# Kernel tuning notes

Measured on AMD Instinct MI355X. Metric: run time of the kernel, lower is better.

Reference implementation:

```python
import jax, jax.numpy as jnp
import numpy as np

B, S, E, H, V, C = 64, 512, 256, 128, 50000, 2


def setup_inputs() -> dict:
    key = jax.random.key(0)
    ks = jax.random.split(key, 12)
    sentences = jax.random.randint(ks[0], (B, S), 0, V, dtype=jnp.int32)
    # sparse binary adjacency (dependency-tree-like), float for bmm
    adj = (jax.random.uniform(ks[1], (B, S, S)) < 0.05).astype(jnp.float32)
    emb_table = jax.random.normal(ks[2], (V, E), dtype=jnp.float32) * 0.02
    W1 = jax.random.normal(ks[3], (H, E), dtype=jnp.float32) * 0.05
    b1 = jnp.zeros((H,), jnp.float32)
    W2 = jax.random.normal(ks[4], (H, H), dtype=jnp.float32) * 0.05
    b2 = jnp.zeros((H,), jnp.float32)
    W3 = jax.random.normal(ks[5], (H, H), dtype=jnp.float32) * 0.05
    b3 = jnp.zeros((H,), jnp.float32)
    Wp = jax.random.normal(ks[6], (C, H), dtype=jnp.float32) * 0.05
    bp = jnp.zeros((C,), jnp.float32)
    return {"sentences": sentences, "adj": adj, "emb_table": emb_table,
            "W1": W1, "b1": b1, "W2": W2, "b2": b2, "W3": W3, "b3": b3,
            "Wp": Wp, "bp": bp}


def reference(sentences, adj, emb_table, W1, b1, W2, b2, W3, b3, Wp, bp):
    # embedding lookup (dropout is eval-mode identity)
    h = emb_table[sentences]  # [B, S, E]
    # degree normalization term (self-loop adds +1)
    deg = jnp.sum(adj, axis=-1, keepdims=True) + 1.0  # [B, S, 1]
    for W, b in ((W1, b1), (W2, b2), (W3, b3)):
        agg = jnp.einsum('bst,btd->bsd', adj, h)  # bmm(adj, h)
        # layer(agg) + layer(h) == (agg + h) @ W^T + 2b  (shared weights)
        h = ((agg + h) @ W.T + 2.0 * b) / deg
        h = jax.nn.relu(h)
    # AdaptiveMaxPool1d(1) over sequence dim
    pooled = jnp.max(h, axis=1)  # [B, H]
    logits = pooled @ Wp.T + bp  # [B, C]
    return logits
```

## Files before the change

### kernel.cpp

```cpp
#include <hip/hip_runtime.h>
#include <hip/hip_bf16.h>

typedef unsigned short ushort_t;

#define B_ 64
#define S_ 512
#define E_ 256
#define H_ 128
#define M_ (B_ * S_)
#define CAP_ 128

__global__ void k_adjidx(const float* __restrict__ adj,
                         ushort_t* __restrict__ idxl,
                         int* __restrict__ nnz,
                         float* __restrict__ invdeg) {
    int row  = blockIdx.x * 4 + (threadIdx.x >> 6);
    int lane = threadIdx.x & 63;
    const float* arow = adj + (size_t)row * S_;
    int total = 0;
    #pragma unroll
    for (int c = 0; c < 8; ++c) {
        float v = arow[c * 64 + lane];
        unsigned long long m = __ballot(v != 0.0f);
        if (v != 0.0f) {
            int pos = total + __popcll(m & ((1ull << lane) - 1ull));
            if (pos < CAP_) idxl[(size_t)row * CAP_ + pos] = (ushort_t)(c * 64 + lane);
        }
        total += __popcll(m);
    }
    if (lane == 0) {
        nnz[row] = total < CAP_ ? total : CAP_;
        invdeg[row] = 1.0f / (float)(total + 1);
    }
}

template <int KDIM, bool GATHER>
__global__ __launch_bounds__(256) void k_gemm(const float* __restrict__ X,
                                              const int* __restrict__ sent,
                                              const float* __restrict__ emb,
                                              const float* __restrict__ W,
                                              float* __restrict__ out) {
    const int BK = 16;
    __shared__ float Xs[BK][68];
    __shared__ float Ws[BK][132];
    int tid = threadIdx.x;
    int rowBlock = blockIdx.x * 64;
    int r0 = (tid >> 5) * 8;
    int c0 = (tid & 31) * 4;
    float acc[8][4] = {};

    int mIdx = tid >> 2;
    int k4   = (tid & 3) * 4;
    const float* xsrc;
    if (GATHER) xsrc = emb + (size_t)sent[rowBlock + mIdx] * KDIM + k4;
    else        xsrc = X   + (size_t)(rowBlock + mIdx) * KDIM + k4;
    int wj = tid >> 1;
    int k8 = (tid & 1) * 8;
    const float* wsrc = W + (size_t)wj * KDIM + k8;

    for (int kk = 0; kk < KDIM; kk += BK) {
        float4 xf = *(const float4*)(xsrc + kk);
        float4 w0 = *(const float4*)(wsrc + kk);
        float4 w1 = *(const float4*)(wsrc + kk + 4);
        Xs[k4 + 0][mIdx] = xf.x; Xs[k4 + 1][mIdx] = xf.y;
        Xs[k4 + 2][mIdx] = xf.z; Xs[k4 + 3][mIdx] = xf.w;
        Ws[k8 + 0][wj] = w0.x; Ws[k8 + 1][wj] = w0.y;
        Ws[k8 + 2][wj] = w0.z; Ws[k8 + 3][wj] = w0.w;
        Ws[k8 + 4][wj] = w1.x; Ws[k8 + 5][wj] = w1.y;
        Ws[k8 + 6][wj] = w1.z; Ws[k8 + 7][wj] = w1.w;
        __syncthreads();
        #pragma unroll
        for (int k = 0; k < BK; ++k) {
            float4 a0 = *(const float4*)&Xs[k][r0];
            float4 a1 = *(const float4*)&Xs[k][r0 + 4];
            float4 wv = *(const float4*)&Ws[k][c0];
            float xv[8] = {a0.x, a0.y, a0.z, a0.w, a1.x, a1.y, a1.z, a1.w};
            #pragma unroll
            for (int i = 0; i < 8; ++i) {
                acc[i][0] += xv[i] * wv.x;
                acc[i][1] += xv[i] * wv.y;
                acc[i][2] += xv[i] * wv.z;
                acc[i][3] += xv[i] * wv.w;
            }
        }
        __syncthreads();
    }

    #pragma unroll
    for (int i = 0; i < 8; ++i) {
        int row = rowBlock + r0 + i;
        float4 o = {acc[i][0], acc[i][1], acc[i][2], acc[i][3]};
        *(float4*)(out + (size_t)row * H_ + c0) = o;
    }
}

__global__ __launch_bounds__(256) void k_aggf(const float* __restrict__ Y,
                                              const ushort_t* __restrict__ idxl,
                                              const int* __restrict__ nnz,
                                              const float* __restrict__ invdeg,
                                              const float* __restrict__ bias,
                                              float* __restrict__ out) {
    int x    = blockIdx.x;
    int xcd  = x & 7;
    int slot = x >> 3;
    int b    = xcd + 8 * (slot >> 6);
    int g    = slot & 63;
    int row  = b * S_ + g * 8 + (threadIdx.x >> 5);
    int c    = threadIdx.x & 31;

    const float4* Y4 = (const float4*)Y;
    int n = nnz[row];
    const ushort_t* il = idxl + (size_t)row * CAP_;
    float4 acc = Y4[(size_t)row * 32 + c];
    float4 acc2 = {0.f, 0.f, 0.f, 0.f};
    size_t base = (size_t)b * S_ * 32;

    int i = 0;
    for (; i + 4 <= n; i += 4) {
        int t0 = il[i], t1 = il[i + 1], t2 = il[i + 2], t3 = il[i + 3];
        float4 v0 = Y4[base + (size_t)t0 * 32 + c];
        float4 v1 = Y4[base + (size_t)t1 * 32 + c];
        float4 v2 = Y4[base + (size_t)t2 * 32 + c];
        float4 v3 = Y4[base + (size_t)t3 * 32 + c];
        acc.x += v0.x + v1.x; acc.y += v0.y + v1.y;
        acc.z += v0.z + v1.z; acc.w += v0.w + v1.w;
        acc2.x += v2.x + v3.x; acc2.y += v2.y + v3.y;
        acc2.z += v2.z + v3.z; acc2.w += v2.w + v3.w;
    }
    for (; i < n; ++i) {
        int t = il[i];
        float4 v = Y4[base + (size_t)t * 32 + c];
        acc.x += v.x; acc.y += v.y; acc.z += v.z; acc.w += v.w;
    }
    acc.x += acc2.x; acc.y += acc2.y; acc.z += acc2.z; acc.w += acc2.w;

    float inv = invdeg[row];
    float4 bv = ((const float4*)bias)[c];
    float4 o;
    o.x = fmaxf((acc.x + 2.0f * bv.x) * inv, 0.0f);
    o.y = fmaxf((acc.y + 2.0f * bv.y) * inv, 0.0f);
    o.z = fmaxf((acc.z + 2.0f * bv.z) * inv, 0.0f);
    o.w = fmaxf((acc.w + 2.0f * bv.w) * inv, 0.0f);
    ((float4*)out)[(size_t)row * 32 + c] = o;
}

__global__ void k_pool(const float* __restrict__ h, float* __restrict__ pp) {
    int b = blockIdx.x, sb = blockIdx.y, j = threadIdx.x;
    const float* p = h + ((size_t)b * S_ + sb * 64) * H_ + j;
    float m = -1e30f;
    #pragma unroll 8
    for (int s = 0; s < 64; ++s) m = fmaxf(m, p[(size_t)s * H_]);
    pp[((size_t)b * 8 + sb) * H_ + j] = m;
}

__global__ void k_final(const float* __restrict__ pp,
                        const float* __restrict__ Wp,
                        const float* __restrict__ bp,
                        float* __restrict__ out) {
    int b = blockIdx.x, j = threadIdx.x;
    float m = -1e30f;
    #pragma unroll
    for (int i = 0; i < 8; ++i) m = fmaxf(m, pp[((size_t)b * 8 + i) * H_ + j]);
    float t0 = m * Wp[j];
    float t1 = m * Wp[H_ + j];
    #pragma unroll
    for (int off = 32; off > 0; off >>= 1) {
        t0 += __shfl_down(t0, off);
        t1 += __shfl_down(t1, off);
    }
    __shared__ float red[2][2];
    int wave = j >> 6, lane = j & 63;
    if (lane == 0) { red[0][wave] = t0; red[1][wave] = t1; }
    __syncthreads();
    if (j == 0) out[b * 2 + 0] = red[0][0] + red[0][1] + bp[0];
    if (j == 1) out[b * 2 + 1] = red[1][0] + red[1][1] + bp[1];
}

extern "C" void kernel_launch(void* const* d_in, const int* in_sizes, int n_in,
                              void* d_out, int out_size, void* d_ws, size_t ws_size,
                              hipStream_t stream) {
    const int*   sent = (const int*)d_in[0];
    const float* adj  = (const float*)d_in[1];
    const float* emb  = (const float*)d_in[2];
    const float* W1   = (const float*)d_in[3];
    const float* b1   = (const float*)d_in[4];
    const float* W2   = (const float*)d_in[5];
    const float* b2   = (const float*)d_in[6];
    const float* W3   = (const float*)d_in[7];
    const float* b3   = (const float*)d_in[8];
    const float* Wp   = (const float*)d_in[9];
    const float* bp   = (const float*)d_in[10];
    float* out = (float*)d_out;

    char* ws = (char*)d_ws;
    float*    bufA   = (float*)ws;
    float*    bufB   = (float*)(ws + (size_t)M_ * 256 * 4);
    float*    invdeg = (float*)(ws + (size_t)M_ * 512 * 4);
    int*      nnz    = (int*)(ws + (size_t)M_ * 512 * 4 + M_ * 4);
    ushort_t* idxl   = (ushort_t*)(ws + (size_t)M_ * 512 * 4 + M_ * 8);
    float*    pp     = (float*)(ws + (size_t)M_ * 512 * 4 + M_ * 8 + (size_t)M_ * CAP_ * 2);

    k_adjidx<<<M_ / 4, 256, 0, stream>>>(adj, idxl, nnz, invdeg);

    k_gemm<E_, true><<<M_ / 64, 256, 0, stream>>>(nullptr, sent, emb, W1, bufA);
    k_aggf<<<M_ / 8, 256, 0, stream>>>(bufA, idxl, nnz, invdeg, b1, bufB);

    k_gemm<H_, false><<<M_ / 64, 256, 0, stream>>>(bufB, nullptr, nullptr, W2, bufA);
    k_aggf<<<M_ / 8, 256, 0, stream>>>(bufA, idxl, nnz, invdeg, b2, bufB);

    k_gemm<H_, false><<<M_ / 64, 256, 0, stream>>>(bufB, nullptr, nullptr, W3, bufA);
    k_aggf<<<M_ / 8, 256, 0, stream>>>(bufA, idxl, nnz, invdeg, b3, bufB);

    k_pool <<<dim3(B_, 8), H_, 0, stream>>>(bufB, pp);
    k_final<<<B_, H_, 0, stream>>>(pp, Wp, bp, out);
}
```

Baseline: 314.3 us.

## Fuse max-pool into final aggregation, double-buffer GEMM smem, vectorize adjacency scan

The last aggregation kernel now reduces each 8-row block to a partial max and writes it directly, so the full layer-3 activations are never stored and the separate pool kernel is removed; the final kernel reduces 64 partials instead of 8. The GEMM uses double-buffered shared memory with register prefetch of the next tile, dropping one barrier per K-step. The adjacency index builder reads float4 per lane instead of scalars. The larger partial buffer requires more workspace, and the register prefetch adds register pressure.

```diff
diff --git a/kernel.cpp b/kernel.cpp
--- a/kernel.cpp
+++ b/kernel.cpp
@@ -16,17 +16,22 @@
                          float* __restrict__ invdeg) {
     int row  = blockIdx.x * 4 + (threadIdx.x >> 6);
     int lane = threadIdx.x & 63;
-    const float* arow = adj + (size_t)row * S_;
+    const float4* arow = (const float4*)(adj + (size_t)row * S_);
+    ushort_t* dst = idxl + (size_t)row * CAP_;
     int total = 0;
     #pragma unroll
-    for (int c = 0; c < 8; ++c) {
-        float v = arow[c * 64 + lane];
-        unsigned long long m = __ballot(v != 0.0f);
-        if (v != 0.0f) {
-            int pos = total + __popcll(m & ((1ull << lane) - 1ull));
-            if (pos < CAP_) idxl[(size_t)row * CAP_ + pos] = (ushort_t)(c * 64 + lane);
-        }
-        total += __popcll(m);
+    for (int c = 0; c < 2; ++c) {
+        float4 v = arow[c * 64 + lane];
+        float f[4] = {v.x, v.y, v.z, v.w};
+        #pragma unroll
+        for (int j = 0; j < 4; ++j) {
+            unsigned long long m = __ballot(f[j] != 0.0f);
+            if (f[j] != 0.0f) {
+                int pos = total + __popcll(m & ((1ull << lane) - 1ull));
+                if (pos < CAP_) dst[pos] = (ushort_t)(c * 256 + lane * 4 + j);
+            }
+            total += __popcll(m);
+        }
     }
     if (lane == 0) {
         nnz[row] = total < CAP_ ? total : CAP_;
@@ -41,8 +46,8 @@
                                               const float* __restrict__ W,
                                               float* __restrict__ out) {
     const int BK = 16;
-    __shared__ float Xs[BK][68];
-    __shared__ float Ws[BK][132];
+    __shared__ float Xs[2][BK][68];
+    __shared__ float Ws[2][BK][132];
     int tid = threadIdx.x;
     int rowBlock = blockIdx.x * 64;
     int r0 = (tid >> 5) * 8;
@@ -58,22 +63,31 @@
     int k8 = (tid & 1) * 8;
     const float* wsrc = W + (size_t)wj * KDIM + k8;
 
-    for (int kk = 0; kk < KDIM; kk += BK) {
-        float4 xf = *(const float4*)(xsrc + kk);
-        float4 w0 = *(const float4*)(wsrc + kk);
-        float4 w1 = *(const float4*)(wsrc + kk + 4);
-        Xs[k4 + 0][mIdx] = xf.x; Xs[k4 + 1][mIdx] = xf.y;
-        Xs[k4 + 2][mIdx] = xf.z; Xs[k4 + 3][mIdx] = xf.w;
-        Ws[k8 + 0][wj] = w0.x; Ws[k8 + 1][wj] = w0.y;
-        Ws[k8 + 2][wj] = w0.z; Ws[k8 + 3][wj] = w0.w;
-        Ws[k8 + 4][wj] = w1.x; Ws[k8 + 5][wj] = w1.y;
-        Ws[k8 + 6][wj] = w1.z; Ws[k8 + 7][wj] = w1.w;
+    float4 xf = *(const float4*)(xsrc);
+    float4 w0 = *(const float4*)(wsrc);
+    float4 w1 = *(const float4*)(wsrc + 4);
+
+    constexpr int NIT = KDIM / BK;
+    #pragma unroll
+    for (int it = 0; it < NIT; ++it) {
+        int buf = it & 1;
+        Xs[buf][k4 + 0][mIdx] = xf.x; Xs[buf][k4 + 1][mIdx] = xf.y;
+        Xs[buf][k4 + 2][mIdx] = xf.z; Xs[buf][k4 + 3][mIdx] = xf.w;
+        Ws[buf][k8 + 0][wj] = w0.x; Ws[buf][k8 + 1][wj] = w0.y;
+        Ws[buf][k8 + 2][wj] = w0.z; Ws[buf][k8 + 3][wj] = w0.w;
+        Ws[buf][k8 + 4][wj] = w1.x; Ws[buf][k8 + 5][wj] = w1.y;
+        Ws[buf][k8 + 6][wj] = w1.z; Ws[buf][k8 + 7][wj] = w1.w;
         __syncthreads();
+        if (it + 1 < NIT) {
+            xf = *(const float4*)(xsrc + (it + 1) * BK);
+            w0 = *(const float4*)(wsrc + (it + 1) * BK);
+            w1 = *(const float4*)(wsrc + (it + 1) * BK + 4);
+        }
         #pragma unroll
         for (int k = 0; k < BK; ++k) {
-            float4 a0 = *(const float4*)&Xs[k][r0];
-            float4 a1 = *(const float4*)&Xs[k][r0 + 4];
-            float4 wv = *(const float4*)&Ws[k][c0];
+            float4 a0 = *(const float4*)&Xs[buf][k][r0];
+            float4 a1 = *(const float4*)&Xs[buf][k][r0 + 4];
+            float4 wv = *(const float4*)&Ws[buf][k][c0];
             float xv[8] = {a0.x, a0.y, a0.z, a0.w, a1.x, a1.y, a1.z, a1.w};
             #pragma unroll
             for (int i = 0; i < 8; ++i) {
@@ -83,7 +97,6 @@
                 acc[i][3] += xv[i] * wv.w;
             }
         }
-        __syncthreads();
     }
 
     #pragma unroll
@@ -94,6 +107,7 @@
     }
 }
 
+template <bool POOL>
 __global__ __launch_bounds__(256) void k_aggf(const float* __restrict__ Y,
                                               const ushort_t* __restrict__ idxl,
                                               const int* __restrict__ nnz,
@@ -105,7 +119,8 @@
     int slot = x >> 3;
     int b    = xcd + 8 * (slot >> 6);
     int g    = slot & 63;
-    int row  = b * S_ + g * 8 + (threadIdx.x >> 5);
+    int r    = threadIdx.x >> 5;
+    int row  = b * S_ + g * 8 + r;
     int c    = threadIdx.x & 31;
 
     const float4* Y4 = (const float4*)Y;
@@ -141,16 +156,24 @@
     o.y = fmaxf((acc.y + 2.0f * bv.y) * inv, 0.0f);
     o.z = fmaxf((acc.z + 2.0f * bv.z) * inv, 0.0f);
     o.w = fmaxf((acc.w + 2.0f * bv.w) * inv, 0.0f);
-    ((float4*)out)[(size_t)row * 32 + c] = o;
-}
-
-__global__ void k_pool(const float* __restrict__ h, float* __restrict__ pp) {
-    int b = blockIdx.x, sb = blockIdx.y, j = threadIdx.x;
-    const float* p = h + ((size_t)b * S_ + sb * 64) * H_ + j;
-    float m = -1e30f;
-    #pragma unroll 8
-    for (int s = 0; s < 64; ++s) m = fmaxf(m, p[(size_t)s * H_]);
-    pp[((size_t)b * 8 + sb) * H_ + j] = m;
+
+    if (!POOL) {
+        ((float4*)out)[(size_t)row * 32 + c] = o;
+    } else {
+        __shared__ float4 sm[8][33];
+        sm[r][c] = o;
+        __syncthreads();
+        if (r == 0) {
+            float4 m = sm[0][c];
+            #pragma unroll
+            for (int q = 1; q < 8; ++q) {
+                float4 v = sm[q][c];
+                m.x = fmaxf(m.x, v.x); m.y = fmaxf(m.y, v.y);
+                m.z = fmaxf(m.z, v.z); m.w = fmaxf(m.w, v.w);
+            }
+            ((float4*)out)[((size_t)b * 64 + g) * 32 + c] = m;
+        }
+    }
 }
 
 __global__ void k_final(const float* __restrict__ pp,
@@ -158,9 +181,10 @@
                         const float* __restrict__ bp,
                         float* __restrict__ out) {
     int b = blockIdx.x, j = threadIdx.x;
+    const float* p = pp + (size_t)b * 64 * H_ + j;
     float m = -1e30f;
-    #pragma unroll
-    for (int i = 0; i < 8; ++i) m = fmaxf(m, pp[((size_t)b * 8 + i) * H_ + j]);
+    #pragma unroll 8
+    for (int i = 0; i < 64; ++i) m = fmaxf(m, p[(size_t)i * H_]);
     float t0 = m * Wp[j];
     float t1 = m * Wp[H_ + j];
     #pragma unroll
@@ -203,14 +227,13 @@
     k_adjidx<<<M_ / 4, 256, 0, stream>>>(adj, idxl, nnz, invdeg);
 
     k_gemm<E_, true><<<M_ / 64, 256, 0, stream>>>(nullptr, sent, emb, W1, bufA);
-    k_aggf<<<M_ / 8, 256, 0, stream>>>(bufA, idxl, nnz, invdeg, b1, bufB);
+    k_aggf<false><<<M_ / 8, 256, 0, stream>>>(bufA, idxl, nnz, invdeg, b1, bufB);
 
     k_gemm<H_, false><<<M_ / 64, 256, 0, stream>>>(bufB, nullptr, nullptr, W2, bufA);
-    k_aggf<<<M_ / 8, 256, 0, stream>>>(bufA, idxl, nnz, invdeg, b2, bufB);
+    k_aggf<false><<<M_ / 8, 256, 0, stream>>>(bufA, idxl, nnz, invdeg, b2, bufB);
 
     k_gemm<H_, false><<<M_ / 64, 256, 0, stream>>>(bufB, nullptr, nullptr, W3, bufA);
-    k_aggf<<<M_ / 8, 256, 0, stream>>>(bufA, idxl, nnz, invdeg, b3, bufB);
-
-    k_pool <<<dim3(B_, 8), H_, 0, stream>>>(bufB, pp);
+    k_aggf<true><<<M_ / 8, 256, 0, stream>>>(bufA, idxl, nnz, invdeg, b3, pp);
+
     k_final<<<B_, H_, 0, stream>>>(pp, Wp, bp, out);
 }
```

Measured after the change: 376.2 us. 1.2x slower.
